# Kernel tuning notes

Hardware: AMD Instinct MI355X
Metric: run time of the kernel (lower is better)

Reference implementation:

```python
import jax, jax.numpy as jnp
import numpy as np

N = 50000        # nodes
E = 800000       # edges
F_IN = 128       # num_feature
NHID = 256
G = 64           # graphs in batch
NUM_GENE = 250
BN_EPS = 1e-5


def setup_inputs() -> dict:
    key = jax.random.key(0)
    ks = jax.random.split(key, 16)
    def w(i, shape, scale=0.05):
        return jax.random.normal(ks[i], shape, dtype=jnp.float32) * scale
    inp = {
        "x": jax.random.normal(ks[0], (N, F_IN), dtype=jnp.float32),
        "edge_index": jax.random.randint(ks[1], (2, E), 0, N, dtype=jnp.int32),
        "batch": jnp.sort(jax.random.randint(ks[2], (N,), 0, G, dtype=jnp.int32)),
        # conv1 MLP (input dim F_IN)
        "w1a": w(3, (F_IN, NHID)), "b1a": jnp.zeros((NHID,), jnp.float32),
        "w1b": w(4, (NHID, NHID)), "b1b": jnp.zeros((NHID,), jnp.float32),
        # convs 2-4 MLPs, stacked [3, ...]
        "W_in": w(5, (3, NHID, NHID)), "b_in": jnp.zeros((3, NHID), jnp.float32),
        "W_out": w(6, (3, NHID, NHID)), "b_out": jnp.zeros((3, NHID), jnp.float32),
        # BatchNorm affine params for bn1..bn4
        "gamma": jnp.ones((4, NHID), jnp.float32),
        "beta": jnp.zeros((4, NHID), jnp.float32),
        # readout head
        "lin1_w": w(7, (2 * NHID, NHID)), "lin1_b": jnp.zeros((NHID,), jnp.float32),
        "lin2_w": w(8, (NHID, NHID // 2)), "lin2_b": jnp.zeros((NHID // 2,), jnp.float32),
        "lin3_w": w(9, (NHID // 2, NUM_GENE)), "lin3_b": jnp.zeros((NUM_GENE,), jnp.float32),
    }
    return inp


def _bn(h, g, b):
    # PyG BatchNorm in training mode: batch statistics over nodes
    mu = h.mean(axis=0)
    var = jnp.mean((h - mu) ** 2, axis=0)
    return g * (h - mu) * jax.lax.rsqrt(var + BN_EPS) + b


def _gin(h, src, dst, W1, c1, W2, c2, g, b):
    # GINConv, eps=0: MLP(x_i + sum_{j->i} x_j), then BN + ReLU
    agg = jax.ops.segment_sum(h[src], dst, num_segments=N)  # [N, d] scatter-sum
    z = h + agg
    z = jnp.maximum(z @ W1 + c1, 0.0) @ W2 + c2
    return jnp.maximum(_bn(z, g, b), 0.0)


def _pool(h, batch):
    # cat([global_max_pool, global_mean_pool]) -> [G, 2*d]
    cnt = jax.ops.segment_sum(jnp.ones((N, 1), h.dtype), batch, num_segments=G)
    gap = jax.ops.segment_sum(h, batch, num_segments=G) / jnp.maximum(cnt, 1.0)
    gmp = jax.ops.segment_max(h, batch, num_segments=G)
    return jnp.concatenate([gmp, gap], axis=1)


def reference(x, edge_index, batch, w1a, b1a, w1b, b1b, W_in, b_in, W_out, b_out,
              gamma, beta, lin1_w, lin1_b, lin2_w, lin2_b, lin3_w, lin3_b):
    src, dst = edge_index[0], edge_index[1]
    h = _gin(x, src, dst, w1a, b1a, w1b, b1b, gamma[0], beta[0])
    acc = _pool(h, batch)
    for i in range(3):  # convs 2-4 (fixed small layer loop)
        h = _gin(h, src, dst, W_in[i], b_in[i], W_out[i], b_out[i], gamma[i + 1], beta[i + 1])
        acc = acc + _pool(h, batch)
    z = jnp.maximum(acc @ lin1_w + lin1_b, 0.0)
    # dropout p=0.5 is identity at inference
    z = jnp.maximum(z @ lin2_w + lin2_b, 0.0)
    y = z @ lin3_w + lin3_b  # [G, NUM_GENE]; torch.squeeze(dim=1) is a no-op here
    return y
```

## Files before the change

kernel.cpp:

```cpp
#include <hip/hip_runtime.h>
#include <hip/hip_bf16.h>

#define GNUM 64
#define BN_EPS 1e-5f

typedef unsigned short u16;
typedef unsigned int u32;
typedef __attribute__((ext_vector_type(8))) short short8;
typedef __attribute__((ext_vector_type(4))) float f32x4;

__device__ inline float bflo(u32 u) { union { u32 i; float f; } v; v.i = u << 16; return v.f; }
__device__ inline float bfhi(u32 u) { union { u32 i; float f; } v; v.i = u & 0xFFFF0000u; return v.f; }
__device__ inline u16 f2bf(float f) {
    union { float f; u32 i; } v; v.f = f;
    u32 x = v.i;
    return (u16)((x + 0x7FFFu + ((x >> 16) & 1u)) >> 16);
}
__device__ inline u32 pack2(float a, float b) { return (u32)f2bf(a) | ((u32)f2bf(b) << 16); }
__device__ inline void acc8(float* a, uint4 v) {
    a[0] += bflo(v.x); a[1] += bfhi(v.x); a[2] += bflo(v.y); a[3] += bfhi(v.y);
    a[4] += bflo(v.z); a[5] += bfhi(v.z); a[6] += bflo(v.w); a[7] += bfhi(v.w);
}

__global__ void zero_f(float* __restrict__ p, int n) {
    int i = blockIdx.x * 256 + threadIdx.x;
    if (i < n) p[i] = 0.f;
}
__global__ void zero_i(int* __restrict__ p, int n) {
    int i = blockIdx.x * 256 + threadIdx.x;
    if (i < n) p[i] = 0;
}

__global__ void deg_kernel(const int* __restrict__ dst, int* __restrict__ deg, int E) {
    int e = blockIdx.x * 256 + threadIdx.x;
    if (e < E) atomicAdd(&deg[dst[e]], 1);
}

__global__ void scan_block(const int* __restrict__ deg, int* __restrict__ part,
                           int* __restrict__ bsum, int n) {
    __shared__ int tmp[256];
    int i = blockIdx.x * 256 + threadIdx.x;
    int v = (i < n) ? deg[i] : 0;
    tmp[threadIdx.x] = v;
    __syncthreads();
    for (int off = 1; off < 256; off <<= 1) {
        int x = 0;
        if (threadIdx.x >= off) x = tmp[threadIdx.x - off];
        __syncthreads();
        tmp[threadIdx.x] += x;
        __syncthreads();
    }
    if (i < n) part[i] = tmp[threadIdx.x];
    if (threadIdx.x == 255) bsum[blockIdx.x] = tmp[255];
}

__global__ void scan_bsum(int* __restrict__ bsum, int nb) {
    __shared__ int tmp[256];
    int v = (threadIdx.x < nb) ? bsum[threadIdx.x] : 0;
    tmp[threadIdx.x] = v;
    __syncthreads();
    for (int off = 1; off < 256; off <<= 1) {
        int x = 0;
        if (threadIdx.x >= off) x = tmp[threadIdx.x - off];
        __syncthreads();
        tmp[threadIdx.x] += x;
        __syncthreads();
    }
    if (threadIdx.x < nb) bsum[threadIdx.x] = tmp[threadIdx.x];
}

__global__ void scan_fix(const int* __restrict__ part, const int* __restrict__ bsum,
                         int* __restrict__ offs, int* __restrict__ cursor, int n) {
    int i = blockIdx.x * 256 + threadIdx.x;
    if (i >= n) return;
    int add = (blockIdx.x > 0) ? bsum[blockIdx.x - 1] : 0;
    int incl = part[i] + add;
    offs[i + 1] = incl;
    cursor[i + 1] = incl;
    if (i == 0) { offs[0] = 0; cursor[0] = 0; }
}

__global__ void fill_kernel(const int* __restrict__ src, const int* __restrict__ dst,
                            int* __restrict__ cursor, int* __restrict__ eidx, int E) {
    int e = blockIdx.x * 256 + threadIdx.x;
    if (e >= E) return;
    int d = dst[e];
    int p = atomicAdd(&cursor[d], 1);
    eidx[p] = src[e];
}

__global__ void cnt_kernel(const int* __restrict__ batch, float* __restrict__ cnt, int Nn) {
    int tid = blockIdx.x * blockDim.x + threadIdx.x;
    int s = tid * 64;
    if (s >= Nn) return;
    int e = min(s + 64, Nn);
    int cur = batch[s]; int run = 0;
    for (int r = s; r < e; ++r) {
        int b = batch[r];
        if (b != cur) { atomicAdd(&cnt[cur], (float)run); cur = b; run = 0; }
        run++;
    }
    atomicAdd(&cnt[cur], (float)run);
}

__global__ void cvt_x(const float* __restrict__ x, u16* __restrict__ xb, int total4) {
    int i = blockIdx.x * 256 + threadIdx.x;
    if (i >= total4) return;
    float4 v = *(const float4*)&x[i * 4];
    uint2 o;
    o.x = pack2(v.x, v.y);
    o.y = pack2(v.z, v.w);
    *(uint2*)&xb[i * 4] = o;
}

template<int K>
__global__ void transw_frag(const float* __restrict__ W, u16* __restrict__ Wp) {
    int o = blockIdx.x * 256 + threadIdx.x;
    if (o >= K * 32) return;
    int l = o & 63;
    int q1 = o >> 6;
    int jf = q1 & 7;
    int q2 = q1 >> 3;
    const int KC = K / 32;
    int kc = q2 & (KC - 1);
    int t = q2 / KC;
    int kbase = kc * 32 + ((l >> 4) << 3);
    int col = t * 128 + jf * 16 + (l & 15);
#pragma unroll
    for (int e = 0; e < 8; ++e)
        Wp[(size_t)o * 8 + e] = f2bf(W[(size_t)(kbase + e) * 256 + col]);
}

template<int F>
__global__ __launch_bounds__(256)
void agg3(const u16* __restrict__ h, const int* __restrict__ offs,
          const int* __restrict__ eidx, u16* __restrict__ z, int Nn) {
    const int CH = F / 8;
    const int G = 64 / CH;
    int lane = threadIdx.x & 63;
    int n = blockIdx.x * 4 + (threadIdx.x >> 6);
    if (n >= Nn) return;
    int cc = lane & (CH - 1);
    int g = lane / CH;
    const u16* hp = h + cc * 8;

    float a[8] = {0.f, 0.f, 0.f, 0.f, 0.f, 0.f, 0.f, 0.f};
    if (g == 0) acc8(a, *(const uint4*)&hp[(size_t)n * F]);

    int j1 = offs[n + 1];
    int j = offs[n] + g;
    for (; j + 3 * G < j1; j += 4 * G) {
        int s0 = eidx[j], s1 = eidx[j + G], s2 = eidx[j + 2 * G], s3 = eidx[j + 3 * G];
        uint4 v0 = *(const uint4*)&hp[(size_t)s0 * F];
        uint4 v1 = *(const uint4*)&hp[(size_t)s1 * F];
        uint4 v2 = *(const uint4*)&hp[(size_t)s2 * F];
        uint4 v3 = *(const uint4*)&hp[(size_t)s3 * F];
        acc8(a, v0); acc8(a, v1); acc8(a, v2); acc8(a, v3);
    }
    for (; j < j1; j += G) {
        uint4 v = *(const uint4*)&hp[(size_t)eidx[j] * F];
        acc8(a, v);
    }
#pragma unroll
    for (int off = 32; off >= CH; off >>= 1)
#pragma unroll
        for (int e = 0; e < 8; ++e) a[e] += __shfl_down(a[e], off, 64);
    if (g == 0) {
        uint4 o;
        o.x = pack2(a[0], a[1]); o.y = pack2(a[2], a[3]);
        o.z = pack2(a[4], a[5]); o.w = pack2(a[6], a[7]);
        *(uint4*)&z[(size_t)n * F + cc * 8] = o;
    }
}

template<int K1>
__global__ __launch_bounds__(256, 2)
void gin_mlp(const u16* __restrict__ Z, const u16* __restrict__ W1p,
             const float* __restrict__ b1, const u16* __restrict__ W2p,
             const float* __restrict__ b2, u16* __restrict__ Cout,
             float* __restrict__ stats, int M) {
    constexpr int KC1 = K1 / 32;
    __shared__ u16 As[64 * K1];
    __shared__ u16 Hs[64 * 256];
    __shared__ u16 tbuf[4608];
    __shared__ float cs[256];
    int t = threadIdx.x;
    int lane = t & 63, wave = t >> 6;
    int m0 = blockIdx.x * 64;
    int lm = lane & 15, q = lane >> 4;

    {
        int row = t >> 2, s = t & 3;
        int gr = m0 + row; if (gr >= M) gr = M - 1;
        const u16* gp = Z + (size_t)gr * K1 + s * (K1 / 4);
        int mf = row >> 4, r15 = row & 15;
#pragma unroll
        for (int j = 0; j < K1 / 32; ++j) {
            uint4 v = *(const uint4*)(gp + j * 8);
            int c = s * (K1 / 32) + j;
            int kc = c >> 2, qq = c & 3;
            *(uint4*)&As[((mf * KC1 + kc) * 64 + r15 + (qq << 4)) * 8] = v;
        }
    }
    __syncthreads();

    f32x4 acc[4][4];
#pragma unroll
    for (int i = 0; i < 4; ++i)
#pragma unroll
        for (int j = 0; j < 4; ++j) acc[i][j] = (f32x4)0.0f;

    {
        const u16* bbase = W1p + ((((size_t)(wave >> 1) * KC1) * 8 + ((wave & 1) << 2)) * 64 + lane) * 8;
        short8 a0[4], a1[4], b0[4], b1r[4];
#pragma unroll
        for (int i = 0; i < 4; ++i) a0[i] = *(const short8*)&As[(i * KC1) * 512 + lane * 8];
#pragma unroll
        for (int j = 0; j < 4; ++j) b0[j] = *(const short8*)(bbase + j * 512);
#pragma unroll
        for (int kc = 0; kc < KC1; ++kc) {
            short8* ac = (kc & 1) ? a1 : a0;
            short8* bc = (kc & 1) ? b1r : b0;
            short8* an = (kc & 1) ? a0 : a1;
            short8* bn = (kc & 1) ? b0 : b1r;
            if (kc + 1 < KC1) {
#pragma unroll
                for (int i = 0; i < 4; ++i)
                    an[i] = *(const short8*)&As[(i * KC1 + kc + 1) * 512 + lane * 8];
#pragma unroll
                for (int j = 0; j < 4; ++j)
                    bn[j] = *(const short8*)(bbase + (size_t)(kc + 1) * 4096 + j * 512);
            }
#pragma unroll
            for (int i = 0; i < 4; ++i)
#pragma unroll
                for (int j = 0; j < 4; ++j)
                    acc[i][j] = __builtin_amdgcn_mfma_f32_16x16x32_bf16(ac[i], bc[j], acc[i][j], 0, 0, 0);
        }
    }

    {
#pragma unroll
        for (int j = 0; j < 4; ++j) {
            float bv = b1[wave * 64 + j * 16 + lm];
            int kc = wave * 2 + (j >> 1);
            int qq = ((j & 1) << 1) + (lm >> 3);
            int e = lm & 7;
#pragma unroll
            for (int i = 0; i < 4; ++i) {
#pragma unroll
                for (int r = 0; r < 4; ++r) {
                    float v = fmaxf(acc[i][j][r] + bv, 0.f);
                    Hs[(((i * 8 + kc) * 64) + (q * 4 + r) + qq * 16) * 8 + e] = f2bf(v);
                }
            }
        }
    }
    __syncthreads();

#pragma unroll
    for (int i = 0; i < 4; ++i)
#pragma unroll
        for (int j = 0; j < 4; ++j) acc[i][j] = (f32x4)0.0f;
    {
        const u16* bbase = W2p + ((((size_t)(wave >> 1) * 8) * 8 + ((wave & 1) << 2)) * 64 + lane) * 8;
        short8 a0[4], a1[4], b0[4], b1r[4];
#pragma unroll
        for (int i = 0; i < 4; ++i) a0[i] = *(const short8*)&Hs[(i * 8) * 512 + lane * 8];
#pragma unroll
        for (int j = 0; j < 4; ++j) b0[j] = *(const short8*)(bbase + j * 512);
#pragma unroll
        for (int kc = 0; kc < 8; ++kc) {
            short8* ac = (kc & 1) ? a1 : a0;
            short8* bc = (kc & 1) ? b1r : b0;
            short8* an = (kc & 1) ? a0 : a1;
            short8* bn = (kc & 1) ? b0 : b1r;
            if (kc + 1 < 8) {
#pragma unroll
                for (int i = 0; i < 4; ++i)
                    an[i] = *(const short8*)&Hs[(i * 8 + kc + 1) * 512 + lane * 8];
#pragma unroll
                for (int j = 0; j < 4; ++j)
                    bn[j] = *(const short8*)(bbase + (size_t)(kc + 1) * 4096 + j * 512);
            }
#pragma unroll
            for (int i = 0; i < 4; ++i)
#pragma unroll
                for (int j = 0; j < 4; ++j)
                    acc[i][j] = __builtin_amdgcn_mfma_f32_16x16x32_bf16(ac[i], bc[j], acc[i][j], 0, 0, 0);
        }
    }

    float bv2[4], s_sum[4], s_sq[4];
#pragma unroll
    for (int j = 0; j < 4; ++j) {
        bv2[j] = b2[wave * 64 + j * 16 + lm];
        s_sum[j] = 0.f; s_sq[j] = 0.f;
    }
#pragma unroll
    for (int i = 0; i < 4; ++i) {
#pragma unroll
        for (int j = 0; j < 4; ++j) {
#pragma unroll
            for (int r = 0; r < 4; ++r) {
                int row = m0 + i * 16 + q * 4 + r;
                float v = acc[i][j][r] + bv2[j];
                if (row < M) { s_sum[j] += v; s_sq[j] = fmaf(v, v, s_sq[j]); }
                tbuf[wave * 1152 + (q * 4 + r) * 72 + j * 16 + lm] = f2bf(v);
            }
        }
        __syncthreads();
        int rl = lane >> 2, seg = lane & 3;
        uint4 w0 = *(const uint4*)&tbuf[wave * 1152 + rl * 72 + seg * 16];
        uint4 w1 = *(const uint4*)&tbuf[wave * 1152 + rl * 72 + seg * 16 + 8];
        int rowg = m0 + i * 16 + rl;
        if (rowg < M) {
            u16* cp = Cout + (size_t)rowg * 256 + wave * 64 + seg * 16;
            *(uint4*)cp = w0;
            *(uint4*)(cp + 8) = w1;
        }
        __syncthreads();
    }

    cs[t] = 0.f;
    __syncthreads();
#pragma unroll
    for (int j = 0; j < 4; ++j) {
        int lc = wave * 64 + j * 16 + lm;
        atomicAdd(&cs[lc], s_sum[j]);
    }
    __syncthreads();
    if (t < 256) atomicAdd(&stats[t], cs[t]);
    __syncthreads();
    cs[t] = 0.f;
    __syncthreads();
#pragma unroll
    for (int j = 0; j < 4; ++j) {
        int lc = wave * 64 + j * 16 + lm;
        atomicAdd(&cs[lc], s_sq[j]);
    }
    __syncthreads();
    if (t < 256) atomicAdd(&stats[256 + t], cs[t]);
}

__global__ __launch_bounds__(256)
void bn_pool(const u16* __restrict__ Z, const float* __restrict__ stats,
             const float* __restrict__ gamma, const float* __restrict__ beta,
             const int* __restrict__ batch, u16* __restrict__ H,
             float* __restrict__ pool_max, float* __restrict__ pool_sum, int Nn) {
    int col = threadIdx.x;
    int r0 = blockIdx.x * 64;
    if (r0 >= Nn) return;
    float mu = stats[col] / (float)Nn;
    float var = stats[256 + col] / (float)Nn - mu * mu;
    float scale = gamma[col] * rsqrtf(var + BN_EPS);
    float shift = beta[col] - mu * scale;
    int rend = min(r0 + 64, Nn);
    int cur = batch[r0];
    float rmax = 0.f, rsum = 0.f;
    for (int r = r0; r < rend; ++r) {
        int bb = batch[r];
        if (bb != cur) {
            atomicMax((int*)&pool_max[cur * 256 + col], __float_as_int(rmax));
            atomicAdd(&pool_sum[cur * 256 + col], rsum);
            cur = bb; rmax = 0.f; rsum = 0.f;
        }
        float v = fmaf(bflo(Z[(size_t)r * 256 + col]), scale, shift);
        v = fmaxf(v, 0.f);
        H[(size_t)r * 256 + col] = f2bf(v);
        rmax = fmaxf(rmax, v); rsum += v;
    }
    atomicMax((int*)&pool_max[cur * 256 + col], __float_as_int(rmax));
    atomicAdd(&pool_sum[cur * 256 + col], rsum);
}

__global__ void acc_update(float* __restrict__ pmax, float* __restrict__ psum,
                           const float* __restrict__ cnt, float* __restrict__ acc,
                           float* __restrict__ stats) {
    int i = blockIdx.x * 256 + threadIdx.x;
    int g = i >> 9, c = i & 511;
    float v;
    if (c < 256) {
        v = pmax[g * 256 + c];
        pmax[g * 256 + c] = 0.f;
    } else {
        int cc = c - 256;
        v = psum[g * 256 + cc] / fmaxf(cnt[g], 1.f);
        psum[g * 256 + cc] = 0.f;
    }
    acc[i] += v;
    if (i < 512) stats[i] = 0.f;
}

__global__ __launch_bounds__(256)
void readout_kernel(const float* __restrict__ acc,
                    const float* __restrict__ w1, const float* __restrict__ b1,
                    const float* __restrict__ w2, const float* __restrict__ b2,
                    const float* __restrict__ w3, const float* __restrict__ b3,
                    float* __restrict__ out) {
    __shared__ float a[512], z1[256], z2[128];
    int g = blockIdx.x, t = threadIdx.x;
    a[t] = acc[g * 512 + t];
    a[t + 256] = acc[g * 512 + 256 + t];
    __syncthreads();
    float s = b1[t];
    for (int k = 0; k < 512; ++k) s = fmaf(a[k], w1[k * 256 + t], s);
    z1[t] = fmaxf(s, 0.f);
    __syncthreads();
    if (t < 128) {
        float s2 = b2[t];
        for (int k = 0; k < 256; ++k) s2 = fmaf(z1[k], w2[k * 128 + t], s2);
        z2[t] = fmaxf(s2, 0.f);
    }
    __syncthreads();
    if (t < 250) {
        float s3 = b3[t];
        for (int k = 0; k < 128; ++k) s3 = fmaf(z2[k], w3[k * 250 + t], s3);
        out[g * 250 + t] = s3;
    }
}

extern "C" void kernel_launch(void* const* d_in, const int* in_sizes, int n_in,
                              void* d_out, int out_size, void* d_ws, size_t ws_size,
                              hipStream_t stream) {
    const float* x     = (const float*)d_in[0];
    const int* ei      = (const int*)d_in[1];
    const int* batch   = (const int*)d_in[2];
    const float* w1a   = (const float*)d_in[3];
    const float* b1a   = (const float*)d_in[4];
    const float* w1b   = (const float*)d_in[5];
    const float* b1b   = (const float*)d_in[6];
    const float* W_in  = (const float*)d_in[7];
    const float* b_in  = (const float*)d_in[8];
    const float* W_out = (const float*)d_in[9];
    const float* b_out = (const float*)d_in[10];
    const float* gamma = (const float*)d_in[11];
    const float* beta  = (const float*)d_in[12];
    const float* l1w   = (const float*)d_in[13];
    const float* l1b   = (const float*)d_in[14];
    const float* l2w   = (const float*)d_in[15];
    const float* l2b   = (const float*)d_in[16];
    const float* l3w   = (const float*)d_in[17];
    const float* l3b   = (const float*)d_in[18];

    const int N = in_sizes[2];
    const int E = in_sizes[1] / 2;
    const int* srcv = ei;
    const int* dstv = ei + E;

    u16* B0 = (u16*)d_ws;
    u16* B1 = B0 + (size_t)N * 256;
    u16* B2 = B1 + (size_t)N * 256;
    u16* Xb = B1;
    u16* Wp = B2 + (size_t)N * 256;
    float* stats = (float*)(Wp + 32768 + 7 * 65536);
    float* pmax  = stats + 512;
    float* psum  = pmax + GNUM * 256;
    float* acc   = psum + GNUM * 256;
    float* cnt   = acc + GNUM * 512;
    int* deg    = (int*)(cnt + GNUM);
    int* part   = deg + N;
    int* bsum   = part + N;
    int* offs   = bsum + 256;
    int* cursor = offs + N + 1;
    int* eidx   = cursor + N + 1;

    int nb256 = (N + 255) / 256;
    int nbM   = (N + 63) / 64;
    int nb64  = (N + 63) / 64;
    int nbW   = (N + 3) / 4;
    int eb    = (E + 255) / 256;
    const int FTOT = 512 + GNUM * 256 * 2 + GNUM * 512 + GNUM;

    zero_i<<<nb256, 256, 0, stream>>>(deg, N);
    zero_f<<<(FTOT + 255) / 256, 256, 0, stream>>>(stats, FTOT);
    deg_kernel<<<eb, 256, 0, stream>>>(dstv, deg, E);
    scan_block<<<nb256, 256, 0, stream>>>(deg, part, bsum, N);
    scan_bsum<<<1, 256, 0, stream>>>(bsum, nb256);
    scan_fix<<<nb256, 256, 0, stream>>>(part, bsum, offs, cursor, N);
    fill_kernel<<<eb, 256, 0, stream>>>(srcv, dstv, cursor, eidx, E);
    cnt_kernel<<<(nb64 + 255) / 256, 256, 0, stream>>>(batch, cnt, N);

    cvt_x<<<(N * 128 / 4 + 255) / 256, 256, 0, stream>>>(x, Xb, N * 128 / 4);
    u16* Wp1 = Wp + 32768;
    transw_frag<128><<<(128 * 32 + 255) / 256, 256, 0, stream>>>(w1a, Wp);
    transw_frag<256><<<(256 * 32 + 255) / 256, 256, 0, stream>>>(w1b, Wp1);
    for (int i = 0; i < 3; ++i) {
        transw_frag<256><<<(256 * 32 + 255) / 256, 256, 0, stream>>>(
            W_in + (size_t)i * 65536, Wp1 + (size_t)(1 + i) * 65536);
        transw_frag<256><<<(256 * 32 + 255) / 256, 256, 0, stream>>>(
            W_out + (size_t)i * 65536, Wp1 + (size_t)(4 + i) * 65536);
    }

    for (int L = 0; L < 4; ++L) {
        if (L == 0) {
            agg3<128><<<nbW, 256, 0, stream>>>(Xb, offs, eidx, B0, N);
            gin_mlp<128><<<nbM, 256, 0, stream>>>(B0, Wp, b1a, Wp1, b1b, B1, stats, N);
            bn_pool<<<nb64, 256, 0, stream>>>(B1, stats, gamma, beta,
                                              batch, B2, pmax, psum, N);
        } else {
            agg3<256><<<nbW, 256, 0, stream>>>(B2, offs, eidx, B0, N);
            gin_mlp<256><<<nbM, 256, 0, stream>>>(
                B0, Wp1 + (size_t)(1 + L - 1) * 65536, b_in + (L - 1) * 256,
                Wp1 + (size_t)(4 + L - 1) * 65536, b_out + (L - 1) * 256, B0, stats, N);
            bn_pool<<<nb64, 256, 0, stream>>>(B0, stats, gamma + L * 256, beta + L * 256,
                                              batch, B2, pmax, psum, N);
        }
        acc_update<<<(GNUM * 512) / 256, 256, 0, stream>>>(pmax, psum, cnt, acc, stats);
    }
    readout_kernel<<<GNUM, 256, 0, stream>>>(acc, l1w, l1b, l2w, l2b, l3w, l3b,
                                             (float*)d_out);
}
```

Measured before the change: 728.4 us.

## Fuse neighbor aggregation into GIN MLP kernel, writing aggregates directly to LDS

Removes the separate agg3 kernel and performs the CSR gather-sum inside the MLP kernel, with each wave aggregating 16 rows straight into the shared-memory A tile. This avoids writing and rereading the aggregated Z buffer through global memory and saves one launch per layer. In exchange the gather now runs inside a kernel limited to two blocks per CU with large LDS, so there is less parallelism to hide the latency of the irregular gather, and the MFMA phase cannot overlap with it. The stats atomic code is also tidied slightly.

```diff
diff --git a/kernel.cpp b/kernel.cpp
--- a/kernel.cpp
+++ b/kernel.cpp
@@ -131,54 +131,13 @@
         Wp[(size_t)o * 8 + e] = f2bf(W[(size_t)(kbase + e) * 256 + col]);
 }
 
-template<int F>
-__global__ __launch_bounds__(256)
-void agg3(const u16* __restrict__ h, const int* __restrict__ offs,
-          const int* __restrict__ eidx, u16* __restrict__ z, int Nn) {
-    const int CH = F / 8;
-    const int G = 64 / CH;
-    int lane = threadIdx.x & 63;
-    int n = blockIdx.x * 4 + (threadIdx.x >> 6);
-    if (n >= Nn) return;
-    int cc = lane & (CH - 1);
-    int g = lane / CH;
-    const u16* hp = h + cc * 8;
-
-    float a[8] = {0.f, 0.f, 0.f, 0.f, 0.f, 0.f, 0.f, 0.f};
-    if (g == 0) acc8(a, *(const uint4*)&hp[(size_t)n * F]);
-
-    int j1 = offs[n + 1];
-    int j = offs[n] + g;
-    for (; j + 3 * G < j1; j += 4 * G) {
-        int s0 = eidx[j], s1 = eidx[j + G], s2 = eidx[j + 2 * G], s3 = eidx[j + 3 * G];
-        uint4 v0 = *(const uint4*)&hp[(size_t)s0 * F];
-        uint4 v1 = *(const uint4*)&hp[(size_t)s1 * F];
-        uint4 v2 = *(const uint4*)&hp[(size_t)s2 * F];
-        uint4 v3 = *(const uint4*)&hp[(size_t)s3 * F];
-        acc8(a, v0); acc8(a, v1); acc8(a, v2); acc8(a, v3);
-    }
-    for (; j < j1; j += G) {
-        uint4 v = *(const uint4*)&hp[(size_t)eidx[j] * F];
-        acc8(a, v);
-    }
-#pragma unroll
-    for (int off = 32; off >= CH; off >>= 1)
-#pragma unroll
-        for (int e = 0; e < 8; ++e) a[e] += __shfl_down(a[e], off, 64);
-    if (g == 0) {
-        uint4 o;
-        o.x = pack2(a[0], a[1]); o.y = pack2(a[2], a[3]);
-        o.z = pack2(a[4], a[5]); o.w = pack2(a[6], a[7]);
-        *(uint4*)&z[(size_t)n * F + cc * 8] = o;
-    }
-}
-
 template<int K1>
 __global__ __launch_bounds__(256, 2)
-void gin_mlp(const u16* __restrict__ Z, const u16* __restrict__ W1p,
-             const float* __restrict__ b1, const u16* __restrict__ W2p,
-             const float* __restrict__ b2, u16* __restrict__ Cout,
-             float* __restrict__ stats, int M) {
+void gin_fused(const u16* __restrict__ Hin, const int* __restrict__ offs,
+               const int* __restrict__ eidx,
+               const u16* __restrict__ W1p, const float* __restrict__ b1,
+               const u16* __restrict__ W2p, const float* __restrict__ b2,
+               u16* __restrict__ Cout, float* __restrict__ stats, int M) {
     constexpr int KC1 = K1 / 32;
     __shared__ u16 As[64 * K1];
     __shared__ u16 Hs[64 * 256];
@@ -190,16 +149,41 @@
     int lm = lane & 15, q = lane >> 4;
 
     {
-        int row = t >> 2, s = t & 3;
-        int gr = m0 + row; if (gr >= M) gr = M - 1;
-        const u16* gp = Z + (size_t)gr * K1 + s * (K1 / 4);
-        int mf = row >> 4, r15 = row & 15;
-#pragma unroll
-        for (int j = 0; j < K1 / 32; ++j) {
-            uint4 v = *(const uint4*)(gp + j * 8);
-            int c = s * (K1 / 32) + j;
-            int kc = c >> 2, qq = c & 3;
-            *(uint4*)&As[((mf * KC1 + kc) * 64 + r15 + (qq << 4)) * 8] = v;
+        const int CH = K1 / 8;
+        const int G = 64 / CH;
+        int cc = lane & (CH - 1);
+        int g = lane / CH;
+        const u16* hp = Hin + cc * 8;
+        for (int rr = 0; rr < 16; ++rr) {
+            int n = m0 + wave * 16 + rr;
+            if (n >= M) n = M - 1;
+            float a[8] = {0.f, 0.f, 0.f, 0.f, 0.f, 0.f, 0.f, 0.f};
+            if (g == 0) acc8(a, *(const uint4*)&hp[(size_t)n * K1]);
+            int j1 = offs[n + 1];
+            int j = offs[n] + g;
+            for (; j + 3 * G < j1; j += 4 * G) {
+                int s0 = eidx[j], s1 = eidx[j + G], s2 = eidx[j + 2 * G], s3 = eidx[j + 3 * G];
+                uint4 v0 = *(const uint4*)&hp[(size_t)s0 * K1];
+                uint4 v1 = *(const uint4*)&hp[(size_t)s1 * K1];
+                uint4 v2 = *(const uint4*)&hp[(size_t)s2 * K1];
+                uint4 v3 = *(const uint4*)&hp[(size_t)s3 * K1];
+                acc8(a, v0); acc8(a, v1); acc8(a, v2); acc8(a, v3);
+            }
+            for (; j < j1; j += G) {
+                uint4 v = *(const uint4*)&hp[(size_t)eidx[j] * K1];
+                acc8(a, v);
+            }
+#pragma unroll
+            for (int off = 32; off >= CH; off >>= 1)
+#pragma unroll
+                for (int e = 0; e < 8; ++e) a[e] += __shfl_down(a[e], off, 64);
+            if (g == 0) {
+                int kc = cc >> 2, qq = cc & 3;
+                uint4 o;
+                o.x = pack2(a[0], a[1]); o.y = pack2(a[2], a[3]);
+                o.z = pack2(a[4], a[5]); o.w = pack2(a[6], a[7]);
+                *(uint4*)&As[((wave * KC1 + kc) * 64 + rr + (qq << 4)) * 8] = o;
+            }
         }
     }
     __syncthreads();
@@ -325,22 +309,18 @@
     cs[t] = 0.f;
     __syncthreads();
 #pragma unroll
-    for (int j = 0; j < 4; ++j) {
-        int lc = wave * 64 + j * 16 + lm;
-        atomicAdd(&cs[lc], s_sum[j]);
-    }
-    __syncthreads();
-    if (t < 256) atomicAdd(&stats[t], cs[t]);
+    for (int j = 0; j < 4; ++j)
+        atomicAdd(&cs[wave * 64 + j * 16 + lm], s_sum[j]);
+    __syncthreads();
+    atomicAdd(&stats[t], cs[t]);
     __syncthreads();
     cs[t] = 0.f;
     __syncthreads();
 #pragma unroll
-    for (int j = 0; j < 4; ++j) {
-        int lc = wave * 64 + j * 16 + lm;
-        atomicAdd(&cs[lc], s_sq[j]);
-    }
-    __syncthreads();
-    if (t < 256) atomicAdd(&stats[256 + t], cs[t]);
+    for (int j = 0; j < 4; ++j)
+        atomicAdd(&cs[wave * 64 + j * 16 + lm], s_sq[j]);
+    __syncthreads();
+    atomicAdd(&stats[256 + t], cs[t]);
 }
 
 __global__ __launch_bounds__(256)
@@ -468,7 +448,6 @@
     int nb256 = (N + 255) / 256;
     int nbM   = (N + 63) / 64;
     int nb64  = (N + 63) / 64;
-    int nbW   = (N + 3) / 4;
     int eb    = (E + 255) / 256;
     const int FTOT = 512 + GNUM * 256 * 2 + GNUM * 512 + GNUM;
 
@@ -494,18 +473,15 @@
 
     for (int L = 0; L < 4; ++L) {
         if (L == 0) {
-            agg3<128><<<nbW, 256, 0, stream>>>(Xb, offs, eidx, B0, N);
-            gin_mlp<128><<<nbM, 256, 0, stream>>>(B0, Wp, b1a, Wp1, b1b, B1, stats, N);
-            bn_pool<<<nb64, 256, 0, stream>>>(B1, stats, gamma, beta,
-                                              batch, B2, pmax, psum, N);
+            gin_fused<128><<<nbM, 256, 0, stream>>>(Xb, offs, eidx,
+                Wp, b1a, Wp1, b1b, B0, stats, N);
         } else {
-            agg3<256><<<nbW, 256, 0, stream>>>(B2, offs, eidx, B0, N);
-            gin_mlp<256><<<nbM, 256, 0, stream>>>(
-                B0, Wp1 + (size_t)(1 + L - 1) * 65536, b_in + (L - 1) * 256,
+            gin_fused<256><<<nbM, 256, 0, stream>>>(B2, offs, eidx,
+                Wp1 + (size_t)(1 + L - 1) * 65536, b_in + (L - 1) * 256,
                 Wp1 + (size_t)(4 + L - 1) * 65536, b_out + (L - 1) * 256, B0, stats, N);
-            bn_pool<<<nb64, 256, 0, stream>>>(B0, stats, gamma + L * 256, beta + L * 256,
-                                              batch, B2, pmax, psum, N);
-        }
+        }
+        bn_pool<<<nb64, 256, 0, stream>>>(B0, stats, gamma + L * 256, beta + L * 256,
+                                          batch, B2, pmax, psum, N);
         acc_update<<<(GNUM * 512) / 256, 256, 0, stream>>>(pmax, psum, cnt, acc, stats);
     }
     readout_kernel<<<GNUM, 256, 0, stream>>>(acc, l1w, l1b, l2w, l2b, l3w, l3b,
```

New measurement: 888.1 us. +21.9%, slower.
